# Performance work log

Measured on AMD Instinct MI355X. Metric: run time of the kernel, lower is better.

## Reference

```python
import jax, jax.numpy as jnp
import numpy as np


def setup_inputs() -> dict:
    key = jax.random.key(0)
    x = jax.random.normal(key, (2, 64, 8192, 1), dtype=jnp.float32)
    return {"x": x}


def pairwise_distance(x):
    # x: (B, N, C) -> (B, N, N) squared euclidean distances
    x_inner = -2.0 * jnp.einsum('bnc,bmc->bnm', x, x)
    x_square = jnp.sum(x * x, axis=-1, keepdims=True)  # (B, N, 1)
    return x_square + x_inner + jnp.swapaxes(x_square, 2, 1)


def reference(x):
    k = 16
    # x: (B, C, N, 1) -> (B, N, C)
    xt = jnp.swapaxes(x, 2, 1).squeeze(-1)
    batch_size, n_points, n_dims = xt.shape
    # top-k of negative distance == k nearest neighbors (self included)
    _, nn_idx = jax.lax.top_k(-pairwise_distance(xt), k)  # (B, N, k)
    center_idx = jnp.broadcast_to(
        jnp.arange(n_points, dtype=nn_idx.dtype)[None, :, None],
        (batch_size, n_points, k),
    )
    return jnp.stack((nn_idx, center_idx), axis=0)  # (2, B, N, k)
```

## Files before the change

### kernel.cpp

```cpp
#include <hip/hip_runtime.h>
#include <cfloat>
#include <climits>

#define NPTS 8192
#define NDIM 64
#define NB   2
#define KK   16
#define NROWS (NB * NPTS)

typedef float f2 __attribute__((ext_vector_type(2)));

__device__ __forceinline__ float np_sum64(const float* v) {
#pragma clang fp contract(off)
    float L[16], M[8], P[4];
#pragma unroll
    for (int l = 0; l < 16; ++l)
        L[l] = __fadd_rn(__fadd_rn(v[l], v[16 + l]), __fadd_rn(v[32 + l], v[48 + l]));
#pragma unroll
    for (int l = 0; l < 8; ++l) M[l] = __fadd_rn(L[l], L[l + 8]);
#pragma unroll
    for (int l = 0; l < 4; ++l) P[l] = __fadd_rn(M[l], M[l + 4]);
    return __fadd_rn(__fadd_rn(P[0], P[2]), __fadd_rn(P[1], P[3]));
}

__global__ __launch_bounds__(256) void k_prep(const float* __restrict__ x,
                                              float* __restrict__ s,
                                              float* __restrict__ xTp) {
#pragma clang fp contract(off)
    int g = blockIdx.x * 256 + threadIdx.x;
    int b = g / NPTS, n = g % NPTS;
    const float* xb = x + (size_t)b * NDIM * NPTS + n;
    float a[NDIM], v[NDIM];
#pragma unroll
    for (int c = 0; c < NDIM; ++c) {
        a[c] = xb[(size_t)c * NPTS];
        v[c] = __fmul_rn(a[c], a[c]);
    }
    s[g] = np_sum64(v);
    float* dst = xTp + ((size_t)(b * NPTS + (n & ~1))) * NDIM + (n & 1);
#pragma unroll
    for (int c = 0; c < NDIM; ++c) dst[2 * c] = a[c];
}

__device__ __forceinline__ f2 pk_mul_blo(f2 a, f2 b) {
    f2 t;
    asm("v_pk_mul_f32 %0, %1, %2 op_sel:[0,0] op_sel_hi:[0,1]"
        : "=v"(t) : "v"(a), "v"(b));
    return t;
}
__device__ __forceinline__ f2 pk_mul_bhi(f2 a, f2 b) {
    f2 t;
    asm("v_pk_mul_f32 %0, %1, %2 op_sel:[1,0] op_sel_hi:[1,1]"
        : "=v"(t) : "v"(a), "v"(b));
    return t;
}
__device__ __forceinline__ void pk_acc(f2& A, f2 t) {
    asm("v_pk_add_f32 %0, %0, %1" : "+v"(A) : "v"(t));
}
__device__ __forceinline__ f2 pk_mul_pl(f2 a, f2 b) {
    f2 t;
    asm("v_pk_mul_f32 %0, %1, %2" : "=v"(t) : "v"(a), "v"(b));
    return t;
}
__device__ __forceinline__ f2 pk_add_pl(f2 a, f2 b) {
    f2 t;
    asm("v_pk_add_f32 %0, %1, %2" : "=v"(t) : "v"(a), "v"(b));
    return t;
}

__global__ __launch_bounds__(256, 1) void k_main(const float* __restrict__ x,
                                                 const float* __restrict__ xTp,
                                                 const float* __restrict__ s,
                                                 float* __restrict__ wd,
                                                 int* __restrict__ wi,
                                                 int js, int jlen) {
#pragma clang fp contract(off)
    const int tid = threadIdx.x;

    const int ngroups = NB * js;
    int group, itile;
    if ((ngroups & 7) == 0) {
        const int gpx  = ngroups >> 3;
        const int xcd  = blockIdx.x & 7;
        const int slot = blockIdx.x >> 3;
        group = xcd * gpx + (slot >> 5);
        itile = slot & 31;
    } else {
        group = blockIdx.x >> 5;
        itile = blockIdx.x & 31;
    }
    const int b     = group / js;
    const int chunk = group - b * js;
    const int i     = itile * 256 + tid;
    const int boff  = b * NPTS;

    __shared__ f2     Bt[32 * 64];
    __shared__ float  ss[64];
    __shared__ float2 buf[8 * 257];

    const float* xb = x + (size_t)b * NDIM * NPTS + i;
    f2 a2[NDIM / 2];
#pragma unroll
    for (int q = 0; q < NDIM / 2; ++q) {
        a2[q].x = xb[(size_t)(2 * q) * NPTS];
        a2[q].y = xb[(size_t)(2 * q + 1) * NPTS];
    }
    const float sif = s[boff + i];
    const f2 si2 = {sif, sif};
    const f2 m2  = {-2.0f, -2.0f};

    float ld[KK]; int li[KK];
#pragma unroll
    for (int e = 0; e < KK; ++e) { ld[e] = FLT_MAX; li[e] = INT_MAX; }
    float ldL = FLT_MAX;
    int   cnt = 0;

    const int j0 = chunk * jlen;
    for (int jt = 0; jt < jlen; jt += 64) {
        __syncthreads();
        {
            const float4* src = (const float4*)(xTp + (size_t)(boff + j0 + jt) * NDIM);
            float4* dstv = (float4*)Bt;
#pragma unroll
            for (int t4 = 0; t4 < 4; ++t4) dstv[t4 * 256 + tid] = src[t4 * 256 + tid];
            if (tid < 16) ((float4*)ss)[tid] = ((const float4*)(s + boff + j0 + jt))[tid];
        }
        __syncthreads();

#pragma unroll 1
        for (int pw = 0; pw < 8; ++pw) {
#pragma unroll
            for (int pp = 0; pp < 4; ++pp) {
                const int p = pw * 4 + pp;
                const float4* bq = (const float4*)&Bt[p * 64];
                f2 A = {0.f, 0.f};
#pragma unroll
                for (int q = 0; q < NDIM / 2; ++q) {
                    float4 B01 = bq[q];
                    f2 B0 = {B01.x, B01.y};
                    f2 B1 = {B01.z, B01.w};
                    pk_acc(A, pk_mul_blo(a2[q], B0));
                    pk_acc(A, pk_mul_bhi(a2[q], B1));
                }
                f2 sj = ((const f2*)ss)[p];
                f2 D  = pk_add_pl(pk_add_pl(si2, pk_mul_pl(m2, A)), sj);
                const int j = j0 + jt + 2 * p;
                if (D.x < ldL) { buf[cnt * 257 + tid] = make_float2(D.x, __int_as_float(j));     cnt++; }
                if (D.y < ldL) { buf[cnt * 257 + tid] = make_float2(D.y, __int_as_float(j + 1)); cnt++; }
            }
            if (__any(cnt > 0)) {
                for (int k = 0; k < cnt; ++k) {
                    float2 e = buf[k * 257 + tid];
                    float cd = e.x; int ci = __float_as_int(e.y);
                    if (cd < ldL) {
#pragma unroll
                        for (int t = 0; t < KK; ++t) {
                            bool sw = cd < ld[t];
                            float od = ld[t]; int oi = li[t];
                            ld[t] = sw ? cd : od;  li[t] = sw ? ci : oi;
                            cd    = sw ? od : cd;  ci    = sw ? oi : ci;
                        }
                        ldL = ld[KK - 1];
                    }
                }
                cnt = 0;
            }
        }
    }

    const int gg = boff + i;
#pragma unroll
    for (int e = 0; e < KK; ++e) {
        wd[(size_t)(chunk * KK + e) * NROWS + gg] = ld[e];
        wi[(size_t)(chunk * KK + e) * NROWS + gg] = li[e];
    }
}

__global__ __launch_bounds__(256) void k_merge(const float* __restrict__ wd,
                                               const int* __restrict__ wi,
                                               int* __restrict__ out,
                                               int js) {
    int g = blockIdx.x * 256 + threadIdx.x;
    int i = g % NPTS;

    float md[KK]; int mi[KK];
#pragma unroll
    for (int e = 0; e < KK; ++e) { md[e] = FLT_MAX; mi[e] = INT_MAX; }

    const int tot = js * KK;
    for (int t = 0; t < tot; ++t) {
        float d  = wd[(size_t)t * NROWS + g];
        int   ix = wi[(size_t)t * NROWS + g];
        bool better = (d < md[KK - 1]) || (d == md[KK - 1] && ix < mi[KK - 1]);
        if (better) {
            float cd = d; int ci = ix;
#pragma unroll
            for (int e = 0; e < KK; ++e) {
                bool sw = (cd < md[e]) || (cd == md[e] && ci < mi[e]);
                float od = md[e]; int oi = mi[e];
                md[e] = sw ? cd : od;  mi[e] = sw ? ci : oi;
                cd    = sw ? od : cd;  ci    = sw ? oi : ci;
            }
        }
    }

    const size_t ob = (size_t)g * KK;
#pragma unroll
    for (int e = 0; e < KK; ++e) {
        out[ob + e] = mi[e];
        out[(size_t)NROWS * KK + ob + e] = i;
    }
}

extern "C" void kernel_launch(void* const* d_in, const int* in_sizes, int n_in,
                              void* d_out, int out_size, void* d_ws, size_t ws_size,
                              hipStream_t stream) {
    const float* x = (const float*)d_in[0];
    int* out = (int*)d_out;

    const size_t S_BYTES  = 65536;
    const size_t XT_BYTES = (size_t)NROWS * NDIM * 4;

    int js = 16;
    while (js > 1) {
        size_t need = S_BYTES + XT_BYTES + (size_t)NROWS * js * KK * 8;
        if (need <= ws_size) break;
        js >>= 1;
    }
    float* s   = (float*)d_ws;
    float* xTp = (float*)((char*)d_ws + S_BYTES);
    float* wd  = (float*)((char*)d_ws + S_BYTES + XT_BYTES);
    int*   wi  = (int*)((char*)d_ws + S_BYTES + XT_BYTES + (size_t)NROWS * js * KK * 4);
    const int jlen = NPTS / js;

    k_prep <<<NROWS / 256, 256, 0, stream>>>(x, s, xTp);
    k_main <<<NB * js * 32, 256, 0, stream>>>(x, xTp, s, wd, wi, js, jlen);
    k_merge<<<NROWS / 256, 256, 0, stream>>>(wd, wi, out, js);
}
```

Measured before the change: 870.1 us.

## Fix split count at compile time and allow two waves per EU in k_main

The split count becomes a compile-time constant of 8 instead of being chosen at runtime from workspace size (up to 16), which halves the k_main grid and doubles the per-block j range. The launch bounds change from one block per CU to amdgpu_waves_per_eu(1,2), and the 32 row registers become named scalars pinned with empty asm so the compiler keeps them in VGPRs. The aim is to let two waves per EU overlap LDS reads and the top-k insertion, and to shorten the merge pass. The risks are register spills under the tighter VGPR budget, fewer blocks to fill the GPU, and a workspace overflow if ws_size is smaller than the fixed layout needs.

```diff
diff --git a/kernel.cpp b/kernel.cpp
--- a/kernel.cpp
+++ b/kernel.cpp
@@ -7,6 +7,7 @@
 #define NB   2
 #define KK   16
 #define NROWS (NB * NPTS)
+#define JS   8
 
 typedef float f2 __attribute__((ext_vector_type(2)));
 
@@ -68,43 +69,52 @@
     return t;
 }
 
-__global__ __launch_bounds__(256, 1) void k_main(const float* __restrict__ x,
-                                                 const float* __restrict__ xTp,
-                                                 const float* __restrict__ s,
-                                                 float* __restrict__ wd,
-                                                 int* __restrict__ wi,
-                                                 int js, int jlen) {
+#define ROW_DECL(q) f2 a2_##q;
+#define ROW_LOAD(q) do { \
+        a2_##q.x = xb[(size_t)(2 * q) * NPTS]; \
+        a2_##q.y = xb[(size_t)(2 * q + 1) * NPTS]; \
+        asm("" : "+v"(a2_##q)); \
+    } while (0);
+#define DOT_STEP(q) do { \
+        float4 B01 = bq[q]; \
+        f2 B0 = {B01.x, B01.y}; \
+        f2 B1 = {B01.z, B01.w}; \
+        pk_acc(A, pk_mul_blo(a2_##q, B0));    \
+        pk_acc(A, pk_mul_bhi(a2_##q, B1));    \
+    } while (0);
+#define REP32(M) M(0) M(1) M(2) M(3) M(4) M(5) M(6) M(7) \
+                 M(8) M(9) M(10) M(11) M(12) M(13) M(14) M(15) \
+                 M(16) M(17) M(18) M(19) M(20) M(21) M(22) M(23) \
+                 M(24) M(25) M(26) M(27) M(28) M(29) M(30) M(31)
+
+__global__ __launch_bounds__(256)
+__attribute__((amdgpu_waves_per_eu(1, 2)))
+void k_main(const float* __restrict__ x,
+            const float* __restrict__ xTp,
+            const float* __restrict__ s,
+            float* __restrict__ wd,
+            int* __restrict__ wi) {
 #pragma clang fp contract(off)
     const int tid = threadIdx.x;
 
-    const int ngroups = NB * js;
-    int group, itile;
-    if ((ngroups & 7) == 0) {
-        const int gpx  = ngroups >> 3;
-        const int xcd  = blockIdx.x & 7;
-        const int slot = blockIdx.x >> 3;
-        group = xcd * gpx + (slot >> 5);
-        itile = slot & 31;
-    } else {
-        group = blockIdx.x >> 5;
-        itile = blockIdx.x & 31;
-    }
-    const int b     = group / js;
-    const int chunk = group - b * js;
+    const int gpx  = (NB * JS) >> 3;
+    const int xcd  = blockIdx.x & 7;
+    const int slot = blockIdx.x >> 3;
+    const int group = xcd * gpx + (slot >> 5);
+    const int itile = slot & 31;
+    const int b     = group / JS;
+    const int chunk = group - b * JS;
     const int i     = itile * 256 + tid;
     const int boff  = b * NPTS;
+    const int jlen  = NPTS / JS;
 
     __shared__ f2     Bt[32 * 64];
     __shared__ float  ss[64];
     __shared__ float2 buf[8 * 257];
 
     const float* xb = x + (size_t)b * NDIM * NPTS + i;
-    f2 a2[NDIM / 2];
-#pragma unroll
-    for (int q = 0; q < NDIM / 2; ++q) {
-        a2[q].x = xb[(size_t)(2 * q) * NPTS];
-        a2[q].y = xb[(size_t)(2 * q + 1) * NPTS];
-    }
+    REP32(ROW_DECL)
+    REP32(ROW_LOAD)
     const float sif = s[boff + i];
     const f2 si2 = {sif, sif};
     const f2 m2  = {-2.0f, -2.0f};
@@ -134,14 +144,7 @@
                 const int p = pw * 4 + pp;
                 const float4* bq = (const float4*)&Bt[p * 64];
                 f2 A = {0.f, 0.f};
-#pragma unroll
-                for (int q = 0; q < NDIM / 2; ++q) {
-                    float4 B01 = bq[q];
-                    f2 B0 = {B01.x, B01.y};
-                    f2 B1 = {B01.z, B01.w};
-                    pk_acc(A, pk_mul_blo(a2[q], B0));
-                    pk_acc(A, pk_mul_bhi(a2[q], B1));
-                }
+                REP32(DOT_STEP)
                 f2 sj = ((const f2*)ss)[p];
                 f2 D  = pk_add_pl(pk_add_pl(si2, pk_mul_pl(m2, A)), sj);
                 const int j = j0 + jt + 2 * p;
@@ -178,8 +181,7 @@
 
 __global__ __launch_bounds__(256) void k_merge(const float* __restrict__ wd,
                                                const int* __restrict__ wi,
-                                               int* __restrict__ out,
-                                               int js) {
+                                               int* __restrict__ out) {
     int g = blockIdx.x * 256 + threadIdx.x;
     int i = g % NPTS;
 
@@ -187,7 +189,7 @@
 #pragma unroll
     for (int e = 0; e < KK; ++e) { md[e] = FLT_MAX; mi[e] = INT_MAX; }
 
-    const int tot = js * KK;
+    const int tot = JS * KK;
     for (int t = 0; t < tot; ++t) {
         float d  = wd[(size_t)t * NROWS + g];
         int   ix = wi[(size_t)t * NROWS + g];
@@ -221,19 +223,12 @@
     const size_t S_BYTES  = 65536;
     const size_t XT_BYTES = (size_t)NROWS * NDIM * 4;
 
-    int js = 16;
-    while (js > 1) {
-        size_t need = S_BYTES + XT_BYTES + (size_t)NROWS * js * KK * 8;
-        if (need <= ws_size) break;
-        js >>= 1;
-    }
     float* s   = (float*)d_ws;
     float* xTp = (float*)((char*)d_ws + S_BYTES);
     float* wd  = (float*)((char*)d_ws + S_BYTES + XT_BYTES);
-    int*   wi  = (int*)((char*)d_ws + S_BYTES + XT_BYTES + (size_t)NROWS * js * KK * 4);
-    const int jlen = NPTS / js;
+    int*   wi  = (int*)((char*)d_ws + S_BYTES + XT_BYTES + (size_t)NROWS * JS * KK * 4);
 
     k_prep <<<NROWS / 256, 256, 0, stream>>>(x, s, xTp);
-    k_main <<<NB * js * 32, 256, 0, stream>>>(x, xTp, s, wd, wi, js, jlen);
-    k_merge<<<NROWS / 256, 256, 0, stream>>>(wd, wi, out, js);
-}
+    k_main <<<NB * JS * 32, 256, 0, stream>>>(x, xTp, s, wd, wi);
+    k_merge<<<NROWS / 256, 256, 0, stream>>>(wd, wi, out);
+}
```

New measurement: 834.1 us. -4.1%, faster.

## Use packed FMA with candidate oversampling and exact refinement pass

Applied to the files above, without the earlier changes.

The main distance loop now uses packed FMA with two independent accumulators instead of a separate multiply and add, roughly halving the VALU instruction count in the dot-product loop. Because FMA changes rounding, each chunk keeps 18 candidates instead of 16. A refine kernel then recomputes the exact non-fused distances for the merged 18 candidates and picks the final top 16. The kernel also drops the occupancy-1 launch bound in favour of 4 waves per EU. The extra candidates add merge work and gather loads, and ranking ties could still differ from the reference in rare cases.

```diff
diff --git a/kernel.cpp b/kernel.cpp
--- a/kernel.cpp
+++ b/kernel.cpp
@@ -6,6 +6,7 @@
 #define NDIM 64
 #define NB   2
 #define KK   16
+#define MM   18
 #define NROWS (NB * NPTS)
 
 typedef float f2 __attribute__((ext_vector_type(2)));
@@ -42,24 +43,17 @@
     for (int c = 0; c < NDIM; ++c) dst[2 * c] = a[c];
 }
 
-__device__ __forceinline__ f2 pk_mul_blo(f2 a, f2 b) {
+__device__ __forceinline__ void pk_fma_blo(f2 a, f2 b, f2& C) {
+    asm("v_pk_fma_f32 %0, %1, %2, %0 op_sel:[0,0,0] op_sel_hi:[0,1,1]"
+        : "+v"(C) : "v"(a), "v"(b));
+}
+__device__ __forceinline__ void pk_fma_bhi(f2 a, f2 b, f2& C) {
+    asm("v_pk_fma_f32 %0, %1, %2, %0 op_sel:[1,0,0] op_sel_hi:[1,1,1]"
+        : "+v"(C) : "v"(a), "v"(b));
+}
+__device__ __forceinline__ f2 pk_fma_pl(f2 a, f2 b, f2 c) {
     f2 t;
-    asm("v_pk_mul_f32 %0, %1, %2 op_sel:[0,0] op_sel_hi:[0,1]"
-        : "=v"(t) : "v"(a), "v"(b));
-    return t;
-}
-__device__ __forceinline__ f2 pk_mul_bhi(f2 a, f2 b) {
-    f2 t;
-    asm("v_pk_mul_f32 %0, %1, %2 op_sel:[1,0] op_sel_hi:[1,1]"
-        : "=v"(t) : "v"(a), "v"(b));
-    return t;
-}
-__device__ __forceinline__ void pk_acc(f2& A, f2 t) {
-    asm("v_pk_add_f32 %0, %0, %1" : "+v"(A) : "v"(t));
-}
-__device__ __forceinline__ f2 pk_mul_pl(f2 a, f2 b) {
-    f2 t;
-    asm("v_pk_mul_f32 %0, %1, %2" : "=v"(t) : "v"(a), "v"(b));
+    asm("v_pk_fma_f32 %0, %1, %2, %3" : "=v"(t) : "v"(a), "v"(b), "v"(c));
     return t;
 }
 __device__ __forceinline__ f2 pk_add_pl(f2 a, f2 b) {
@@ -68,13 +62,32 @@
     return t;
 }
 
-__global__ __launch_bounds__(256, 1) void k_main(const float* __restrict__ x,
-                                                 const float* __restrict__ xTp,
-                                                 const float* __restrict__ s,
-                                                 float* __restrict__ wd,
-                                                 int* __restrict__ wi,
-                                                 int js, int jlen) {
-#pragma clang fp contract(off)
+#define ROW_DECL(q) f2 a2_##q;
+#define ROW_LOAD(q) do { \
+        a2_##q.x = xb[(size_t)(2 * q) * NPTS]; \
+        a2_##q.y = xb[(size_t)(2 * q + 1) * NPTS]; \
+        asm("" : "+v"(a2_##q)); \
+    } while (0);
+#define FMA_STEP(q) do { \
+        float4 B01 = bq[q]; \
+        f2 B0 = {B01.x, B01.y}; \
+        f2 B1 = {B01.z, B01.w}; \
+        pk_fma_blo(a2_##q, B0, Aa);    \
+        pk_fma_bhi(a2_##q, B1, Ab);    \
+    } while (0);
+#define REP32(M) M(0) M(1) M(2) M(3) M(4) M(5) M(6) M(7) \
+                 M(8) M(9) M(10) M(11) M(12) M(13) M(14) M(15) \
+                 M(16) M(17) M(18) M(19) M(20) M(21) M(22) M(23) \
+                 M(24) M(25) M(26) M(27) M(28) M(29) M(30) M(31)
+
+__global__ __launch_bounds__(256)
+__attribute__((amdgpu_waves_per_eu(4, 4)))
+void k_phase1(const float* __restrict__ x,
+              const float* __restrict__ xTp,
+              const float* __restrict__ s,
+              float* __restrict__ wd,
+              int* __restrict__ wi,
+              int js, int jlen) {
     const int tid = threadIdx.x;
 
     const int ngroups = NB * js;
@@ -99,19 +112,15 @@
     __shared__ float2 buf[8 * 257];
 
     const float* xb = x + (size_t)b * NDIM * NPTS + i;
-    f2 a2[NDIM / 2];
-#pragma unroll
-    for (int q = 0; q < NDIM / 2; ++q) {
-        a2[q].x = xb[(size_t)(2 * q) * NPTS];
-        a2[q].y = xb[(size_t)(2 * q + 1) * NPTS];
-    }
+    REP32(ROW_DECL)
+    REP32(ROW_LOAD)
     const float sif = s[boff + i];
     const f2 si2 = {sif, sif};
     const f2 m2  = {-2.0f, -2.0f};
 
-    float ld[KK]; int li[KK];
-#pragma unroll
-    for (int e = 0; e < KK; ++e) { ld[e] = FLT_MAX; li[e] = INT_MAX; }
+    float ld[MM]; int li[MM];
+#pragma unroll
+    for (int e = 0; e < MM; ++e) { ld[e] = FLT_MAX; li[e] = INT_MAX; }
     float ldL = FLT_MAX;
     int   cnt = 0;
 
@@ -133,17 +142,12 @@
             for (int pp = 0; pp < 4; ++pp) {
                 const int p = pw * 4 + pp;
                 const float4* bq = (const float4*)&Bt[p * 64];
-                f2 A = {0.f, 0.f};
-#pragma unroll
-                for (int q = 0; q < NDIM / 2; ++q) {
-                    float4 B01 = bq[q];
-                    f2 B0 = {B01.x, B01.y};
-                    f2 B1 = {B01.z, B01.w};
-                    pk_acc(A, pk_mul_blo(a2[q], B0));
-                    pk_acc(A, pk_mul_bhi(a2[q], B1));
-                }
-                f2 sj = ((const f2*)ss)[p];
-                f2 D  = pk_add_pl(pk_add_pl(si2, pk_mul_pl(m2, A)), sj);
+                f2 Aa = {0.f, 0.f}, Ab = {0.f, 0.f};
+                REP32(FMA_STEP)
+                f2 A   = pk_add_pl(Aa, Ab);
+                f2 sj  = ((const f2*)ss)[p];
+                f2 sij = pk_add_pl(si2, sj);
+                f2 D   = pk_fma_pl(m2, A, sij);
                 const int j = j0 + jt + 2 * p;
                 if (D.x < ldL) { buf[cnt * 257 + tid] = make_float2(D.x, __int_as_float(j));     cnt++; }
                 if (D.y < ldL) { buf[cnt * 257 + tid] = make_float2(D.y, __int_as_float(j + 1)); cnt++; }
@@ -154,13 +158,13 @@
                     float cd = e.x; int ci = __float_as_int(e.y);
                     if (cd < ldL) {
 #pragma unroll
-                        for (int t = 0; t < KK; ++t) {
+                        for (int t = 0; t < MM; ++t) {
                             bool sw = cd < ld[t];
                             float od = ld[t]; int oi = li[t];
                             ld[t] = sw ? cd : od;  li[t] = sw ? ci : oi;
                             cd    = sw ? od : cd;  ci    = sw ? oi : ci;
                         }
-                        ldL = ld[KK - 1];
+                        ldL = ld[MM - 1];
                     }
                 }
                 cnt = 0;
@@ -170,32 +174,35 @@
 
     const int gg = boff + i;
 #pragma unroll
-    for (int e = 0; e < KK; ++e) {
-        wd[(size_t)(chunk * KK + e) * NROWS + gg] = ld[e];
-        wi[(size_t)(chunk * KK + e) * NROWS + gg] = li[e];
-    }
-}
-
-__global__ __launch_bounds__(256) void k_merge(const float* __restrict__ wd,
-                                               const int* __restrict__ wi,
-                                               int* __restrict__ out,
-                                               int js) {
-    int g = blockIdx.x * 256 + threadIdx.x;
-    int i = g % NPTS;
-
-    float md[KK]; int mi[KK];
-#pragma unroll
-    for (int e = 0; e < KK; ++e) { md[e] = FLT_MAX; mi[e] = INT_MAX; }
-
-    const int tot = js * KK;
+    for (int e = 0; e < MM; ++e) {
+        wd[(size_t)(chunk * MM + e) * NROWS + gg] = ld[e];
+        wi[(size_t)(chunk * MM + e) * NROWS + gg] = li[e];
+    }
+}
+
+__global__ __launch_bounds__(256) void k_refine(const float* __restrict__ x,
+                                                const float* __restrict__ s,
+                                                const float* __restrict__ wd,
+                                                const int* __restrict__ wi,
+                                                int* __restrict__ out,
+                                                int js) {
+#pragma clang fp contract(off)
+    const int g = blockIdx.x * 256 + threadIdx.x;
+    const int b = g / NPTS, i = g % NPTS;
+    const float* xb = x + (size_t)b * NDIM * NPTS;
+
+    float md[MM]; int mi[MM];
+#pragma unroll
+    for (int e = 0; e < MM; ++e) { md[e] = FLT_MAX; mi[e] = INT_MAX; }
+    const int tot = js * MM;
     for (int t = 0; t < tot; ++t) {
         float d  = wd[(size_t)t * NROWS + g];
         int   ix = wi[(size_t)t * NROWS + g];
-        bool better = (d < md[KK - 1]) || (d == md[KK - 1] && ix < mi[KK - 1]);
+        bool better = (d < md[MM - 1]) || (d == md[MM - 1] && ix < mi[MM - 1]);
         if (better) {
             float cd = d; int ci = ix;
 #pragma unroll
-            for (int e = 0; e < KK; ++e) {
+            for (int e = 0; e < MM; ++e) {
                 bool sw = (cd < md[e]) || (cd == md[e] && ci < mi[e]);
                 float od = md[e]; int oi = mi[e];
                 md[e] = sw ? cd : od;  mi[e] = sw ? ci : oi;
@@ -204,10 +211,45 @@
         }
     }
 
+    float dot[MM];
+#pragma unroll
+    for (int t = 0; t < MM; ++t) dot[t] = 0.f;
+    for (int c = 0; c < NDIM; ++c) {
+        const float* row = xb + (size_t)c * NPTS;
+        float xic = row[i];
+#pragma unroll
+        for (int t = 0; t < MM; ++t)
+            dot[t] = __fadd_rn(dot[t], __fmul_rn(xic, row[mi[t]]));
+    }
+    const float si = s[b * NPTS + i];
+    float de[MM];
+#pragma unroll
+    for (int t = 0; t < MM; ++t)
+        de[t] = __fadd_rn(__fadd_rn(si, __fmul_rn(-2.0f, dot[t])), s[b * NPTS + mi[t]]);
+
+    float fd[KK]; int fi[KK];
+#pragma unroll
+    for (int e = 0; e < KK; ++e) { fd[e] = FLT_MAX; fi[e] = INT_MAX; }
+#pragma unroll
+    for (int t = 0; t < MM; ++t) {
+        float d = de[t]; int ix = mi[t];
+        bool better = (d < fd[KK - 1]) || (d == fd[KK - 1] && ix < fi[KK - 1]);
+        if (better) {
+            float cd = d; int ci = ix;
+#pragma unroll
+            for (int e = 0; e < KK; ++e) {
+                bool sw = (cd < fd[e]) || (cd == fd[e] && ci < fi[e]);
+                float od = fd[e]; int oi = fi[e];
+                fd[e] = sw ? cd : od;  fi[e] = sw ? ci : oi;
+                cd    = sw ? od : cd;  ci    = sw ? oi : ci;
+            }
+        }
+    }
+
     const size_t ob = (size_t)g * KK;
 #pragma unroll
     for (int e = 0; e < KK; ++e) {
-        out[ob + e] = mi[e];
+        out[ob + e] = fi[e];
         out[(size_t)NROWS * KK + ob + e] = i;
     }
 }
@@ -223,17 +265,17 @@
 
     int js = 16;
     while (js > 1) {
-        size_t need = S_BYTES + XT_BYTES + (size_t)NROWS * js * KK * 8;
+        size_t need = S_BYTES + XT_BYTES + (size_t)NROWS * js * MM * 8;
         if (need <= ws_size) break;
         js >>= 1;
     }
     float* s   = (float*)d_ws;
     float* xTp = (float*)((char*)d_ws + S_BYTES);
     float* wd  = (float*)((char*)d_ws + S_BYTES + XT_BYTES);
-    int*   wi  = (int*)((char*)d_ws + S_BYTES + XT_BYTES + (size_t)NROWS * js * KK * 4);
+    int*   wi  = (int*)((char*)d_ws + S_BYTES + XT_BYTES + (size_t)NROWS * js * MM * 4);
     const int jlen = NPTS / js;
 
-    k_prep <<<NROWS / 256, 256, 0, stream>>>(x, s, xTp);
-    k_main <<<NB * js * 32, 256, 0, stream>>>(x, xTp, s, wd, wi, js, jlen);
-    k_merge<<<NROWS / 256, 256, 0, stream>>>(wd, wi, out, js);
-}
+    k_prep  <<<NROWS / 256, 256, 0, stream>>>(x, s, xTp);
+    k_phase1<<<NB * js * 32, 256, 0, stream>>>(x, xTp, s, wd, wi, js, jlen);
+    k_refine<<<NROWS / 256, 256, 0, stream>>>(x, s, wd, wi, out, js);
+}
```

Result: faster. 828.5 us (-4.8%).
